# Optimization experiments

Measured on AMD Instinct MI355X. Metric: run time of the kernel, lower is better.

The kernel has to match this reference:

```python
import jax, jax.numpy as jnp
import numpy as np

N, E = 50000, 800000
NODE_DIM, EDGE_DIM, HEADS = 64, 16, 4
C = NODE_DIM // HEADS  # per-head channels
NEG_SLOPE = 0.2
BN_EPS = 1e-5


def setup_inputs() -> dict:
    key = jax.random.key(0)
    ks = jax.random.split(key, 12)
    glorot = lambda k, shape: jax.random.normal(k, shape, jnp.float32) * np.sqrt(2.0 / (shape[0] + shape[-1]))
    return {
        "x": jax.random.normal(ks[0], (N, NODE_DIM), jnp.float32),
        "edge_index": jax.random.randint(ks[1], (2, E), 0, N, jnp.int32),
        "edge_attr": jax.random.normal(ks[2], (E, EDGE_DIM), jnp.float32),
        "W_l": glorot(ks[3], (NODE_DIM, HEADS * C)),
        "b_l": jnp.zeros((HEADS * C,), jnp.float32),
        "W_r": glorot(ks[4], (NODE_DIM, HEADS * C)),
        "b_r": jnp.zeros((HEADS * C,), jnp.float32),
        "W_e": glorot(ks[5], (EDGE_DIM, HEADS * C)),
        "att": glorot(ks[6], (HEADS, C)),
        "bias": jnp.zeros((HEADS * C,), jnp.float32),
        "gamma": jnp.ones((NODE_DIM,), jnp.float32),
        "beta": jnp.zeros((NODE_DIM,), jnp.float32),
    }


def reference(x, edge_index, edge_attr, W_l, b_l, W_r, b_r, W_e, att, bias, gamma, beta):
    src, dst = edge_index[0], edge_index[1]
    n = x.shape[0]
    # GATv2: node transforms for source (l) and target (r) roles
    xl = (x @ W_l + b_l).reshape(n, HEADS, C)
    xr = (x @ W_r + b_r).reshape(n, HEADS, C)
    e = (edge_attr @ W_e).reshape(-1, HEADS, C)
    # per-edge attention logits: leaky_relu(x_j + x_i + e) . att  -> [E, H]
    g = jax.nn.leaky_relu(xl[src] + xr[dst] + e, NEG_SLOPE)
    logits = jnp.einsum('ehc,hc->eh', g, att)
    # segment softmax grouped by destination node
    amax = jax.ops.segment_max(logits, dst, num_segments=n)
    ex = jnp.exp(logits - amax[dst])
    denom = jax.ops.segment_sum(ex, dst, num_segments=n)
    alpha = ex / (denom[dst] + 1e-16)  # [E, H]
    # weighted message aggregation (scatter-add over dst), concat heads
    msg = xl[src] * alpha[..., None]  # [E, H, C]
    out = jax.ops.segment_sum(msg, dst, num_segments=n).reshape(n, HEADS * C) + bias
    # BatchNorm (training-mode batch statistics over nodes)
    mean = out.mean(axis=0)
    var = out.var(axis=0)
    out = (out - mean) * jax.lax.rsqrt(var + BN_EPS) * gamma + beta
    # residual + exact GELU
    return jax.nn.gelu(out + x, approximate=False)
```

## Files before the change

### kernel.cpp

```cpp
#include <hip/hip_runtime.h>
#include <hip/hip_fp16.h>
#include <math.h>

#define NODE_DIM 64
#define EDGE_DIM 16
#define CAP 64
#define NEG_SLOPE 0.2f
#define BN_EPS 1e-5f

typedef unsigned short ushort_t;
typedef unsigned int uint_t;

template<int CTRL>
__device__ __forceinline__ float dpp_mov_f(float v) {
    return __int_as_float(__builtin_amdgcn_update_dpp(
        0, __float_as_int(v), CTRL, 0xF, 0xF, true));
}
__device__ __forceinline__ float row_sum16(float v) {
    v += dpp_mov_f<0x128>(v);
    v += dpp_mov_f<0x124>(v);
    v += dpp_mov_f<0x122>(v);
    v += dpp_mov_f<0x121>(v);
    return v;
}
__device__ __forceinline__ float wave_sum64(float v) {
    v = row_sum16(v);
    v += __shfl_xor(v, 16, 64);
    v += __shfl_xor(v, 32, 64);
    return v;
}
__device__ __forceinline__ float wave_max64(float v) {
    v = fmaxf(v, dpp_mov_f<0x128>(v));
    v = fmaxf(v, dpp_mov_f<0x124>(v));
    v = fmaxf(v, dpp_mov_f<0x122>(v));
    v = fmaxf(v, dpp_mov_f<0x121>(v));
    v = fmaxf(v, __shfl_xor(v, 16, 64));
    v = fmaxf(v, __shfl_xor(v, 32, 64));
    return v;
}
__device__ __forceinline__ ushort_t f2bf(float f) {
    unsigned int b = __float_as_uint(f);
    b += 0x7FFFu + ((b >> 16) & 1u);
    return (ushort_t)(b >> 16);
}
__device__ __forceinline__ float bf2f(ushort_t u) {
    return __uint_as_float(((unsigned int)u) << 16);
}
__device__ __forceinline__ uint_t packh2(float a, float b) {
    __half2 h;
    h.x = __float2half_rn(a);
    h.y = __float2half_rn(b);
    return *reinterpret_cast<uint_t*>(&h);
}
__device__ __forceinline__ float2 unpackh2(uint_t u) {
    __half2 h = *reinterpret_cast<__half2*>(&u);
    return make_float2(__half2float(h.x), __half2float(h.y));
}

__global__ __launch_bounds__(256) void k_transform(
    const float* __restrict__ x, const float* __restrict__ Wl,
    const float* __restrict__ bl, const float* __restrict__ Wr,
    const float* __restrict__ br, ushort_t* __restrict__ xlbf,
    ushort_t* __restrict__ xrbf, int n)
{
    __shared__ float sWl[NODE_DIM * NODE_DIM];
    __shared__ float sWr[NODE_DIM * NODE_DIM];
    for (int i = threadIdx.x; i < NODE_DIM * NODE_DIM; i += 256) {
        sWl[i] = Wl[i];
        sWr[i] = Wr[i];
    }
    __syncthreads();
    int lane = threadIdx.x & 63;
    int wid = threadIdx.x >> 6;
    for (int row = blockIdx.x * 4 + wid; row < n; row += gridDim.x * 4) {
        float xown = x[(size_t)row * NODE_DIM + lane];
        float al = bl[lane], ar = br[lane];
#pragma unroll
        for (int k = 0; k < NODE_DIM; k++) {
            float xv = __shfl(xown, k, 64);
            al = fmaf(xv, sWl[k * 64 + lane], al);
            ar = fmaf(xv, sWr[k * 64 + lane], ar);
        }
        xlbf[(size_t)row * NODE_DIM + lane] = f2bf(al);
        xrbf[(size_t)row * NODE_DIM + lane] = f2bf(ar);
    }
}

__global__ __launch_bounds__(256) void k_edge(
    const int* __restrict__ ei, const float* __restrict__ eattr,
    const float* __restrict__ We, const float* __restrict__ att,
    int* __restrict__ cursors,
    const ushort_t* __restrict__ xlbf, const ushort_t* __restrict__ xrbf,
    int* __restrict__ slots, uint4* __restrict__ payload, int E)
{
    __shared__ float sea[4][64 * EDGE_DIM];
    __shared__ float slg[4][64 * 4];

    int lane = threadIdx.x & 63;
    int wid = threadIdx.x >> 6;
    int wbase = (blockIdx.x * 4 + wid) * 64;
    if (wbase >= E) return;
    wbase = __builtin_amdgcn_readfirstlane(wbase);
    int cnt = E - wbase; if (cnt > 64) cnt = 64;

    {
        const float4* esrc = (const float4*)(eattr + (size_t)wbase * EDGE_DIM);
        float4* sdst = (float4*)sea[wid];
        int lim = cnt * 4;
#pragma unroll
        for (int r = 0; r < 4; r++) {
            int idx = r * 64 + lane;
            if (idx < lim) sdst[idx] = esrc[idx];
        }
    }

    float we_c[EDGE_DIM];
#pragma unroll
    for (int k = 0; k < EDGE_DIM; k++) we_c[k] = We[k * NODE_DIM + lane];
    float att_p = att[lane];
    float att_n = att_p * NEG_SLOPE;

    int src_l = 0;
    if (lane < cnt) {
        src_l = ei[wbase + lane];
        int dst_l = ei[E + wbase + lane];
        int pos_l = atomicAdd(&cursors[dst_l], 1);
        if (pos_l < CAP) slots[(size_t)dst_l * CAP + pos_l] = wbase + lane;
    }
    int dst_l_bc = (lane < cnt) ? ei[E + wbase + lane] : 0;

    float* seaW = sea[wid];
    float* slgW = slg[wid];

    ushort_t pxl[8], pxr[8];
    auto LOADT = [&](int t, int k) {
        int s = __builtin_amdgcn_readlane(src_l, t);
        int d = __builtin_amdgcn_readlane(dst_l_bc, t);
        pxl[k] = xlbf[(size_t)s * NODE_DIM + lane];
        pxr[k] = xrbf[(size_t)d * NODE_DIM + lane];
    };
    auto COMP = [&](int t, int k) {
        const float4* e4 = (const float4*)(seaW + t * EDGE_DIM);
        float4 a0 = e4[0], a1 = e4[1], a2 = e4[2], a3 = e4[3];
        float p0 = 0.f, p1 = 0.f;
        p0 = fmaf(a0.x, we_c[0], p0);  p1 = fmaf(a0.y, we_c[1], p1);
        p0 = fmaf(a0.z, we_c[2], p0);  p1 = fmaf(a0.w, we_c[3], p1);
        p0 = fmaf(a1.x, we_c[4], p0);  p1 = fmaf(a1.y, we_c[5], p1);
        p0 = fmaf(a1.z, we_c[6], p0);  p1 = fmaf(a1.w, we_c[7], p1);
        p0 = fmaf(a2.x, we_c[8], p0);  p1 = fmaf(a2.y, we_c[9], p1);
        p0 = fmaf(a2.z, we_c[10], p0); p1 = fmaf(a2.w, we_c[11], p1);
        p0 = fmaf(a3.x, we_c[12], p0); p1 = fmaf(a3.y, we_c[13], p1);
        p0 = fmaf(a3.z, we_c[14], p0); p1 = fmaf(a3.w, we_c[15], p1);
        float sv = bf2f(pxl[k]) + bf2f(pxr[k]) + (p0 + p1);
        float g = sv * (sv > 0.f ? att_p : att_n);
        g = row_sum16(g);
        if ((lane & 15) == 0) slgW[t * 4 + (lane >> 4)] = g;
    };

    if (cnt == 64) {
#pragma unroll
        for (int k = 0; k < 8; k++) LOADT(k, k);
#pragma unroll 1
        for (int tb = 0; tb < 56; tb += 8) {
#pragma unroll
            for (int k = 0; k < 8; k++) {
                COMP(tb + k, k);
                LOADT(tb + k + 8, k);
            }
        }
#pragma unroll
        for (int k = 0; k < 8; k++) COMP(56 + k, k);
    } else {
#pragma unroll
        for (int k = 0; k < 8; k++) if (k < cnt) LOADT(k, k);
        for (int tb = 0; tb < cnt; tb += 8) {
#pragma unroll
            for (int k = 0; k < 8; k++) {
                int t = tb + k;
                if (t < cnt) {
                    COMP(t, k);
                    int tn = t + 8;
                    if (tn < cnt) LOADT(tn, k);
                }
            }
        }
    }

    if (lane < cnt) {
        float4 lg4 = ((const float4*)slgW)[lane];
        payload[wbase + lane] =
            make_uint4((uint_t)src_l, packh2(lg4.x, lg4.y),
                       packh2(lg4.z, lg4.w), 0u);
    }
}

__global__ __launch_bounds__(256) void k_fused(
    const int* __restrict__ slots, const uint4* __restrict__ payload,
    const int* __restrict__ cursors, const ushort_t* __restrict__ xlbf,
    const float* __restrict__ bias, float* __restrict__ out, int n)
{
    __shared__ float salpha[4][CAP * 4];
    __shared__ int ssrc[4][CAP];

    int wid = threadIdx.x >> 6;
    int lane = threadIdx.x & 63;
    int i = blockIdx.x * 4 + wid;
    if (i >= n) return;

    int deg = cursors[i];
    if (deg > CAP) deg = CAP;
    bool act = (lane < deg);

    int eid = act ? slots[(size_t)i * CAP + lane] : 0;
    uint4 pl = act ? payload[eid] : make_uint4(0u, 0u, 0u, 0u);
    int se_x = (int)pl.x;
    float2 g01 = unpackh2(pl.y);
    float2 g23 = unpackh2(pl.z);

    float l0 = act ? g01.x : -1e30f;
    float l1 = act ? g01.y : -1e30f;
    float l2 = act ? g23.x : -1e30f;
    float l3 = act ? g23.y : -1e30f;
    float m0 = wave_max64(l0), m1 = wave_max64(l1);
    float m2 = wave_max64(l2), m3 = wave_max64(l3);
    float e0 = act ? __expf(l0 - m0) : 0.f;
    float e1 = act ? __expf(l1 - m1) : 0.f;
    float e2 = act ? __expf(l2 - m2) : 0.f;
    float e3 = act ? __expf(l3 - m3) : 0.f;
    float s0 = wave_sum64(e0), s1 = wave_sum64(e1);
    float s2 = wave_sum64(e2), s3 = wave_sum64(e3);
    float* salW = salpha[wid];
    int* ssrcW = ssrc[wid];
    ((float4*)salW)[lane] = make_float4(
        e0 / (s0 + 1e-16f), e1 / (s1 + 1e-16f),
        e2 / (s2 + 1e-16f), e3 / (s3 + 1e-16f));
    ssrcW[lane] = se_x;

    int r = lane >> 3, c = lane & 7;
    float a0 = 0.f, a1 = 0.f, a2 = 0.f, a3 = 0.f;
    float a4 = 0.f, a5 = 0.f, a6 = 0.f, a7 = 0.f;
    int nb = (deg + 7) >> 3;
    for (int b = 0; b < nb; b++) {
        int t = b * 8 + r;
        int src_t = ssrcW[t];
        float al = salW[t * 4 + (c >> 1)];
        uint4 v = *(const uint4*)(xlbf + (size_t)src_t * NODE_DIM + c * 8);
        a0 = fmaf(al, __uint_as_float(v.x << 16), a0);
        a1 = fmaf(al, __uint_as_float(v.x & 0xFFFF0000u), a1);
        a2 = fmaf(al, __uint_as_float(v.y << 16), a2);
        a3 = fmaf(al, __uint_as_float(v.y & 0xFFFF0000u), a3);
        a4 = fmaf(al, __uint_as_float(v.z << 16), a4);
        a5 = fmaf(al, __uint_as_float(v.z & 0xFFFF0000u), a5);
        a6 = fmaf(al, __uint_as_float(v.w << 16), a6);
        a7 = fmaf(al, __uint_as_float(v.w & 0xFFFF0000u), a7);
    }
#define RED(x) do { \
        x += dpp_mov_f<0x128>(x); \
        x += __shfl_xor(x, 16, 64); \
        x += __shfl_xor(x, 32, 64); } while (0)
    RED(a0); RED(a1); RED(a2); RED(a3);
    RED(a4); RED(a5); RED(a6); RED(a7);
#undef RED
    float t0 = (r & 1) ? a1 : a0;
    float t1 = (r & 1) ? a3 : a2;
    float t2 = (r & 1) ? a5 : a4;
    float t3 = (r & 1) ? a7 : a6;
    float u0 = (r & 2) ? t1 : t0;
    float u1 = (r & 2) ? t3 : t2;
    float w  = (r & 4) ? u1 : u0;
    int ch = c * 8 + r;
    out[(size_t)i * NODE_DIM + ch] = w + bias[ch];
}

__global__ __launch_bounds__(256) void k_bnstat(
    const float* __restrict__ out, float* __restrict__ stats, int n)
{
    __shared__ float sbuf[256];
    int col = threadIdx.x & 63;
    int rgrp = threadIdx.x >> 6;
    float s = 0.f, q = 0.f;
    for (int row = blockIdx.x * 4 + rgrp; row < n; row += gridDim.x * 4) {
        float v = out[(size_t)row * 64 + col];
        s += v;
        q = fmaf(v, v, q);
    }
    sbuf[threadIdx.x] = s;
    __syncthreads();
    if (threadIdx.x < 64) {
        s = sbuf[threadIdx.x] + sbuf[threadIdx.x + 64] +
            sbuf[threadIdx.x + 128] + sbuf[threadIdx.x + 192];
        atomicAdd(&stats[col], s);
    }
    __syncthreads();
    sbuf[threadIdx.x] = q;
    __syncthreads();
    if (threadIdx.x < 64) {
        q = sbuf[threadIdx.x] + sbuf[threadIdx.x + 64] +
            sbuf[threadIdx.x + 128] + sbuf[threadIdx.x + 192];
        atomicAdd(&stats[64 + col], q);
    }
}

__global__ __launch_bounds__(256) void k_final(
    float* __restrict__ out, const float* __restrict__ x,
    const float* __restrict__ stats, const float* __restrict__ gamma,
    const float* __restrict__ beta, int total, float invn)
{
    int i = blockIdx.x * 256 + threadIdx.x;
    if (i >= total) return;
    int c = i & 63;
    float mean = stats[c] * invn;
    float var = stats[64 + c] * invn - mean * mean;
    float z = (out[i] - mean) * rsqrtf(var + BN_EPS) * gamma[c] + beta[c] + x[i];
    out[i] = z * 0.5f * (1.f + erff(z * 0.70710678118654752f));
}

extern "C" void kernel_launch(void* const* d_in, const int* in_sizes, int n_in,
                              void* d_out, int out_size, void* d_ws, size_t ws_size,
                              hipStream_t stream)
{
    const float* x     = (const float*)d_in[0];
    const int*   ei    = (const int*)d_in[1];
    const float* eattr = (const float*)d_in[2];
    const float* Wl    = (const float*)d_in[3];
    const float* bl    = (const float*)d_in[4];
    const float* Wr    = (const float*)d_in[5];
    const float* br    = (const float*)d_in[6];
    const float* We    = (const float*)d_in[7];
    const float* att   = (const float*)d_in[8];
    const float* bias  = (const float*)d_in[9];
    const float* gamma = (const float*)d_in[10];
    const float* beta  = (const float*)d_in[11];
    int n = in_sizes[0] / NODE_DIM;
    int E = in_sizes[1] / 2;

    char* ws = (char*)d_ws;
    ushort_t* xlbf    = (ushort_t*)ws; ws += (size_t)n * NODE_DIM * 2;
    ushort_t* xrbf    = (ushort_t*)ws; ws += (size_t)n * NODE_DIM * 2;
    uint4*    payload = (uint4*)ws;    ws += (size_t)E * 16;
    int*      slots   = (int*)ws;      ws += (size_t)n * CAP * 4;
    int*      cursors = (int*)ws;      ws += (size_t)n * 4;
    float*    stats   = (float*)ws;    ws += 128 * 4;

    hipMemsetAsync(cursors, 0, (size_t)(n + 128) * 4, stream);

    k_transform<<<512, 256, 0, stream>>>(x, Wl, bl, Wr, br, xlbf, xrbf, n);
    k_edge<<<(E + 255) / 256, 256, 0, stream>>>(
        ei, eattr, We, att, cursors, xlbf, xrbf, slots, payload, E);
    k_fused<<<(n + 3) / 4, 256, 0, stream>>>(
        slots, payload, cursors, xlbf, bias, (float*)d_out, n);
    k_bnstat<<<256, 256, 0, stream>>>((const float*)d_out, stats, n);
    k_final<<<(n * NODE_DIM + 255) / 256, 256, 0, stream>>>(
        (float*)d_out, x, stats, gamma, beta, n * NODE_DIM, 1.0f / n);
}
```

Before: 180.5 us.

## Use packed fp16 dot2 for node and edge projections, keep logits in registers

The node transform now keeps the W_l/W_r columns as packed fp16 pairs in registers and accumulates with v_dot2 fp16 instructions, replacing the LDS-staged fp32 FMA loop. The edge kernel drops its LDS staging of edge attributes: each lane holds its own edge's attributes as packed halves, which are broadcast via readlane and fed to dot2 against packed W_e. In the full-wave path the logits stay in registers and are transposed with two xor-shuffles instead of an LDS round trip. The transform grid size is also doubled. The cost is lower precision from fp16 rounding of inputs and weights, plus higher register pressure from the fully unrolled 64-edge loop.

```diff
diff --git a/kernel.cpp b/kernel.cpp
--- a/kernel.cpp
+++ b/kernel.cpp
@@ -10,6 +10,7 @@
 
 typedef unsigned short ushort_t;
 typedef unsigned int uint_t;
+typedef __fp16 h2_t __attribute__((ext_vector_type(2)));
 
 template<int CTRL>
 __device__ __forceinline__ float dpp_mov_f(float v) {
@@ -56,6 +57,16 @@
     __half2 h = *reinterpret_cast<__half2*>(&u);
     return make_float2(__half2float(h.x), __half2float(h.y));
 }
+__device__ __forceinline__ float fdot2u(uint_t a, uint_t b, float c) {
+#if __has_builtin(__builtin_amdgcn_fdot2)
+    union { uint_t u; h2_t h; } ua, ub;
+    ua.u = a; ub.u = b;
+    return __builtin_amdgcn_fdot2(ua.h, ub.h, c, false);
+#else
+    float2 fa = unpackh2(a), fb = unpackh2(b);
+    return fmaf(fa.y, fb.y, fmaf(fa.x, fb.x, c));
+#endif
+}
 
 __global__ __launch_bounds__(256) void k_transform(
     const float* __restrict__ x, const float* __restrict__ Wl,
@@ -63,23 +74,31 @@
     const float* __restrict__ br, ushort_t* __restrict__ xlbf,
     ushort_t* __restrict__ xrbf, int n)
 {
-    __shared__ float sWl[NODE_DIM * NODE_DIM];
-    __shared__ float sWr[NODE_DIM * NODE_DIM];
-    for (int i = threadIdx.x; i < NODE_DIM * NODE_DIM; i += 256) {
-        sWl[i] = Wl[i];
-        sWr[i] = Wr[i];
-    }
-    __syncthreads();
     int lane = threadIdx.x & 63;
     int wid = threadIdx.x >> 6;
+
+    uint_t wlp[32], wrp[32];
+#pragma unroll
+    for (int m = 0; m < 32; m++) {
+        wlp[m] = packh2(Wl[(2 * m) * NODE_DIM + lane],
+                        Wl[(2 * m + 1) * NODE_DIM + lane]);
+        wrp[m] = packh2(Wr[(2 * m) * NODE_DIM + lane],
+                        Wr[(2 * m + 1) * NODE_DIM + lane]);
+    }
+    float blc = bl[lane], brc = br[lane];
+
     for (int row = blockIdx.x * 4 + wid; row < n; row += gridDim.x * 4) {
-        float xown = x[(size_t)row * NODE_DIM + lane];
-        float al = bl[lane], ar = br[lane];
-#pragma unroll
-        for (int k = 0; k < NODE_DIM; k++) {
-            float xv = __shfl(xown, k, 64);
-            al = fmaf(xv, sWl[k * 64 + lane], al);
-            ar = fmaf(xv, sWr[k * 64 + lane], ar);
+        const float4* x4 = (const float4*)(x + (size_t)row * NODE_DIM);
+        float al = blc, ar = brc;
+#pragma unroll
+        for (int p = 0; p < 16; p++) {
+            float4 v = x4[p];
+            uint_t x01 = packh2(v.x, v.y);
+            uint_t x23 = packh2(v.z, v.w);
+            al = fdot2u(x01, wlp[2 * p], al);
+            al = fdot2u(x23, wlp[2 * p + 1], al);
+            ar = fdot2u(x01, wrp[2 * p], ar);
+            ar = fdot2u(x23, wrp[2 * p + 1], ar);
         }
         xlbf[(size_t)row * NODE_DIM + lane] = f2bf(al);
         xrbf[(size_t)row * NODE_DIM + lane] = f2bf(ar);
@@ -93,7 +112,6 @@
     const ushort_t* __restrict__ xlbf, const ushort_t* __restrict__ xrbf,
     int* __restrict__ slots, uint4* __restrict__ payload, int E)
 {
-    __shared__ float sea[4][64 * EDGE_DIM];
     __shared__ float slg[4][64 * 4];
 
     int lane = threadIdx.x & 63;
@@ -103,20 +121,26 @@
     wbase = __builtin_amdgcn_readfirstlane(wbase);
     int cnt = E - wbase; if (cnt > 64) cnt = 64;
 
+    uint_t eap[8];
     {
-        const float4* esrc = (const float4*)(eattr + (size_t)wbase * EDGE_DIM);
-        float4* sdst = (float4*)sea[wid];
-        int lim = cnt * 4;
-#pragma unroll
-        for (int r = 0; r < 4; r++) {
-            int idx = r * 64 + lane;
-            if (idx < lim) sdst[idx] = esrc[idx];
-        }
-    }
-
-    float we_c[EDGE_DIM];
-#pragma unroll
-    for (int k = 0; k < EDGE_DIM; k++) we_c[k] = We[k * NODE_DIM + lane];
+        const float4* e4 = (const float4*)(eattr + (size_t)(wbase + lane) * EDGE_DIM);
+        bool ld = lane < cnt;
+        float4 z = make_float4(0.f, 0.f, 0.f, 0.f);
+        float4 v0 = ld ? e4[0] : z;
+        float4 v1 = ld ? e4[1] : z;
+        float4 v2 = ld ? e4[2] : z;
+        float4 v3 = ld ? e4[3] : z;
+        eap[0] = packh2(v0.x, v0.y); eap[1] = packh2(v0.z, v0.w);
+        eap[2] = packh2(v1.x, v1.y); eap[3] = packh2(v1.z, v1.w);
+        eap[4] = packh2(v2.x, v2.y); eap[5] = packh2(v2.z, v2.w);
+        eap[6] = packh2(v3.x, v3.y); eap[7] = packh2(v3.z, v3.w);
+    }
+
+    uint_t wep[8];
+#pragma unroll
+    for (int m = 0; m < 8; m++)
+        wep[m] = packh2(We[(2 * m) * NODE_DIM + lane],
+                        We[(2 * m + 1) * NODE_DIM + lane]);
     float att_p = att[lane];
     float att_n = att_p * NEG_SLOPE;
 
@@ -128,9 +152,6 @@
         if (pos_l < CAP) slots[(size_t)dst_l * CAP + pos_l] = wbase + lane;
     }
     int dst_l_bc = (lane < cnt) ? ei[E + wbase + lane] : 0;
-
-    float* seaW = sea[wid];
-    float* slgW = slg[wid];
 
     ushort_t pxl[8], pxr[8];
     auto LOADT = [&](int t, int k) {
@@ -139,58 +160,71 @@
         pxl[k] = xlbf[(size_t)s * NODE_DIM + lane];
         pxr[k] = xrbf[(size_t)d * NODE_DIM + lane];
     };
-    auto COMP = [&](int t, int k) {
-        const float4* e4 = (const float4*)(seaW + t * EDGE_DIM);
-        float4 a0 = e4[0], a1 = e4[1], a2 = e4[2], a3 = e4[3];
-        float p0 = 0.f, p1 = 0.f;
-        p0 = fmaf(a0.x, we_c[0], p0);  p1 = fmaf(a0.y, we_c[1], p1);
-        p0 = fmaf(a0.z, we_c[2], p0);  p1 = fmaf(a0.w, we_c[3], p1);
-        p0 = fmaf(a1.x, we_c[4], p0);  p1 = fmaf(a1.y, we_c[5], p1);
-        p0 = fmaf(a1.z, we_c[6], p0);  p1 = fmaf(a1.w, we_c[7], p1);
-        p0 = fmaf(a2.x, we_c[8], p0);  p1 = fmaf(a2.y, we_c[9], p1);
-        p0 = fmaf(a2.z, we_c[10], p0); p1 = fmaf(a2.w, we_c[11], p1);
-        p0 = fmaf(a3.x, we_c[12], p0); p1 = fmaf(a3.y, we_c[13], p1);
-        p0 = fmaf(a3.z, we_c[14], p0); p1 = fmaf(a3.w, we_c[15], p1);
-        float sv = bf2f(pxl[k]) + bf2f(pxr[k]) + (p0 + p1);
-        float g = sv * (sv > 0.f ? att_p : att_n);
-        g = row_sum16(g);
-        if ((lane & 15) == 0) slgW[t * 4 + (lane >> 4)] = g;
+    auto EPROJ = [&](int t) {
+        float p = 0.f;
+#pragma unroll
+        for (int m = 0; m < 8; m++) {
+            uint_t ea = (uint_t)__builtin_amdgcn_readlane((int)eap[m], t);
+            p = fdot2u(ea, wep[m], p);
+        }
+        return p;
     };
 
     if (cnt == 64) {
+        float kp[4];
+        auto COMPF = [&](int t, int k, int j) {
+            float p = EPROJ(t);
+            float sv = bf2f(pxl[k]) + bf2f(pxr[k]) + p;
+            float g = sv * (sv > 0.f ? att_p : att_n);
+            g = row_sum16(g);
+            if ((lane & 15) == (t & 15)) kp[j] = g;
+        };
 #pragma unroll
         for (int k = 0; k < 8; k++) LOADT(k, k);
-#pragma unroll 1
-        for (int tb = 0; tb < 56; tb += 8) {
-#pragma unroll
-            for (int k = 0; k < 8; k++) {
-                COMP(tb + k, k);
-                LOADT(tb + k + 8, k);
-            }
-        }
-#pragma unroll
-        for (int k = 0; k < 8; k++) COMP(56 + k, k);
+#pragma unroll
+        for (int t = 0; t < 64; t++) {
+            COMPF(t, t & 7, t >> 4);
+            if (t + 8 < 64) LOADT(t + 8, (t + 8) & 7);
+        }
+        int h4 = lane >> 4;
+        float xA = (h4 & 1) ? kp[0] : kp[1];
+        float yA = (h4 & 1) ? kp[2] : kp[3];
+        xA = __shfl_xor(xA, 16, 64);
+        yA = __shfl_xor(yA, 16, 64);
+        float A0 = (h4 & 1) ? xA : kp[0];
+        float A1 = (h4 & 1) ? kp[1] : xA;
+        float A2 = (h4 & 1) ? yA : kp[2];
+        float A3 = (h4 & 1) ? kp[3] : yA;
+        float xB = (h4 & 2) ? A0 : A2;
+        float yB = (h4 & 2) ? A1 : A3;
+        xB = __shfl_xor(xB, 32, 64);
+        yB = __shfl_xor(yB, 32, 64);
+        float B0 = (h4 & 2) ? xB : A0;
+        float B1 = (h4 & 2) ? yB : A1;
+        float B2 = (h4 & 2) ? A2 : xB;
+        float B3 = (h4 & 2) ? A3 : yB;
+        payload[wbase + lane] =
+            make_uint4((uint_t)src_l, packh2(B0, B1), packh2(B2, B3), 0u);
     } else {
-#pragma unroll
-        for (int k = 0; k < 8; k++) if (k < cnt) LOADT(k, k);
-        for (int tb = 0; tb < cnt; tb += 8) {
-#pragma unroll
-            for (int k = 0; k < 8; k++) {
-                int t = tb + k;
-                if (t < cnt) {
-                    COMP(t, k);
-                    int tn = t + 8;
-                    if (tn < cnt) LOADT(tn, k);
-                }
-            }
-        }
-    }
-
-    if (lane < cnt) {
-        float4 lg4 = ((const float4*)slgW)[lane];
-        payload[wbase + lane] =
-            make_uint4((uint_t)src_l, packh2(lg4.x, lg4.y),
-                       packh2(lg4.z, lg4.w), 0u);
+        float* slgW = slg[wid];
+        for (int t = 0; t < cnt; t++) {
+            int s = __builtin_amdgcn_readlane(src_l, t);
+            int d = __builtin_amdgcn_readlane(dst_l_bc, t);
+            ushort_t xlv = xlbf[(size_t)s * NODE_DIM + lane];
+            ushort_t xrv = xrbf[(size_t)d * NODE_DIM + lane];
+            float p = EPROJ(t);
+            float sv = bf2f(xlv) + bf2f(xrv) + p;
+            float g = sv * (sv > 0.f ? att_p : att_n);
+            g = row_sum16(g);
+            if ((lane & 15) == 0) slgW[t * 4 + (lane >> 4)] = g;
+        }
+        __builtin_amdgcn_s_waitcnt(0);
+        if (lane < cnt) {
+            float4 lg4 = ((const float4*)slgW)[lane];
+            payload[wbase + lane] =
+                make_uint4((uint_t)src_l, packh2(lg4.x, lg4.y),
+                           packh2(lg4.z, lg4.w), 0u);
+        }
     }
 }
 
@@ -344,7 +378,7 @@
 
     hipMemsetAsync(cursors, 0, (size_t)(n + 128) * 4, stream);
 
-    k_transform<<<512, 256, 0, stream>>>(x, Wl, bl, Wr, br, xlbf, xrbf, n);
+    k_transform<<<1024, 256, 0, stream>>>(x, Wl, bl, Wr, br, xlbf, xrbf, n);
     k_edge<<<(E + 255) / 256, 256, 0, stream>>>(
         ei, eattr, We, att, cursors, xlbf, xrbf, slots, payload, E);
     k_fused<<<(n + 3) / 4, 256, 0, stream>>>(
```

Measured after the change: 193.5 us. +7.2%, slower.
